# Performance work log

Hardware: AMD Instinct MI355X
Metric: run time of the kernel (lower is better)

The kernel has to match this reference:

```python
import jax, jax.numpy as jnp
import numpy as np

S, B, C = 7, 2, 20
N = B * 5 + C  # 30
L_COORD, L_NOOBJ = 5.0, 0.5


def setup_inputs() -> dict:
    key = jax.random.key(0)
    k1, k2, k3, k4 = jax.random.split(key, 4)
    batch = 16384
    pred = jax.random.uniform(k1, (batch, S, S, N), dtype=jnp.float32)
    target = jax.random.uniform(k2, (batch, S, S, N), dtype=jnp.float32)
    # rescale w/h channels of both boxes to [0.5, 1) so the (buggy) in-place
    # coordinate transform never yields negative values under sqrt
    wh_idx = jnp.array([2, 3, 7, 8])
    pred = pred.at[..., wh_idx].set(0.5 + 0.5 * pred[..., wh_idx])
    target = target.at[..., wh_idx].set(0.5 + 0.5 * target[..., wh_idx])
    obj = jax.random.uniform(k3, (batch, S, S)) < 0.25
    conf = 0.1 + 0.9 * jax.random.uniform(k4, (batch, S, S))
    target = target.at[..., 4].set(jnp.where(obj, conf, 0.0))
    return {"pred": pred, "target": target}


def _yolo_loss(pred, target):
    # Faithful vectorization of the original loop-y torch forward, bugs included:
    #  * x2y2 is computed from the ALREADY transformed xy (xy_new/S + 0.5*wh)
    #  * lambda_coord only multiplies the x / sqrt(w) terms, not y / sqrt(h)
    #  * the selected per-cell loss SUMS l1+l2+l3+IoU (IoU itself is added)
    #  * only the first min(S^2, #coord_cells) coord cells (global flatten
    #    order across the batch) contribute to bbox_loss
    #  * class-prob loss slices dim1 of a [M,2,5] tensor with 10: -> empty -> 0
    p = pred.reshape(-1, N)   # [M, 30], M = b*S*S, row-major like torch mask gather
    t = target.reshape(-1, N)
    obj = t[:, 4] > 0
    rank = jnp.cumsum(obj.astype(jnp.int32)) - 1  # rank among coord cells
    active = obj & (rank < S * S)                 # cells whose bbox loss counts

    pb = p[:, :10].reshape(-1, B, 5)  # [M, B, 5]
    tb = t[:, :10].reshape(-1, B, 5)

    def transform(box):
        xy = box[..., :2] / S - 0.5 * box[..., 2:4]      # new x1,y1
        x2y2 = xy / S + 0.5 * box[..., 2:4]              # uses NEW xy (original bug)
        return xy, x2y2

    pxy, p2 = transform(pb)
    txy, t2 = transform(tb)

    l1 = L_COORD * (txy[..., 0] - pxy[..., 0]) ** 2 + (txy[..., 1] - pxy[..., 1]) ** 2
    l2 = (L_COORD * (jnp.sqrt(t2[..., 0]) - jnp.sqrt(p2[..., 0])) ** 2
          + (jnp.sqrt(t2[..., 1]) - jnp.sqrt(p2[..., 1])) ** 2)
    l3 = (tb[..., 4] - pb[..., 4]) ** 2

    # IoU between pred box j and target box j (boxes as [x1,y1,x2,y2])
    lt = jnp.maximum(pxy, txy)
    rb = jnp.minimum(p2, t2)
    wh = jnp.maximum(rb - lt, 0.0)
    inter = wh[..., 0] * wh[..., 1]
    area_p = (p2[..., 0] - pxy[..., 0]) * (p2[..., 1] - pxy[..., 1])
    area_t = (t2[..., 0] - txy[..., 0]) * (t2[..., 1] - txy[..., 1])
    iou = inter / (area_p + area_t - inter)  # [M, B]

    tot = l1 + l2 + l3 + iou                 # sum(info[argmax]) includes IoU
    jstar = jnp.argmax(iou, axis=1)          # responsible box per cell
    sel = jnp.take_along_axis(tot, jstar[:, None], axis=1)[:, 0]
    bbox_loss = jnp.sum(jnp.where(active, sel, 0.0))

    # no-object confidence loss over both boxes' conf channels (4 and 9)
    noobj = ~obj
    conf_sq = (p[:, 4] - t[:, 4]) ** 2 + (p[:, 9] - t[:, 9]) ** 2
    noobj_loss = L_NOOBJ * jnp.sum(jnp.where(noobj, conf_sq, 0.0))

    # class prob loss: original slices [:, 10:] on a [M, B, 5] tensor -> empty -> 0
    class_prob_loss = jnp.float32(0.0)

    return bbox_loss + noobj_loss + class_prob_loss


def reference(pred, target):
    return _yolo_loss(pred, target)
```

## Files before the change

kernel.cpp:

```cpp
#include <hip/hip_runtime.h>

#define NCH 30
#define RANK_LIMIT 49
#define L_COORD 5.0f
#define L_NOOBJ 0.5f

#define NB 980
#define UNROLL 4
#define OUTER 6
#define CHUNK (256 * UNROLL)
#define NBLK_TOTAL (NB + 1)

typedef float vfloat4 __attribute__((ext_vector_type(4)));

__device__ inline float block_reduce(float v) {
    #pragma unroll
    for (int off = 32; off > 0; off >>= 1)
        v += __shfl_down(v, off, 64);
    __shared__ float s[4];
    int lane = threadIdx.x & 63, wid = threadIdx.x >> 6;
    if (lane == 0) s[wid] = v;
    __syncthreads();
    return (threadIdx.x == 0) ? (s[0] + s[1] + s[2] + s[3]) : 0.0f;
}

__device__ inline float sel_loss(const float* __restrict__ p,
                                 const float* __restrict__ t, int row) {
    const float invS = 1.0f / 7.0f;
    int b0 = row * NCH;
    float tot0 = 0.f, tot1 = 0.f, iou0 = 0.f, iou1 = 0.f;
    #pragma unroll
    for (int j = 0; j < 2; ++j) {
        int o = b0 + 5 * j;
        float px = p[o + 0], py = p[o + 1], pw = p[o + 2], ph = p[o + 3], pc = p[o + 4];
        float tx = t[o + 0], ty = t[o + 1], tw = t[o + 2], th = t[o + 3], tc = t[o + 4];
        float pxy0 = px * invS - 0.5f * pw;
        float pxy1 = py * invS - 0.5f * ph;
        float p2x  = pxy0 * invS + 0.5f * pw;
        float p2y  = pxy1 * invS + 0.5f * ph;
        float txy0 = tx * invS - 0.5f * tw;
        float txy1 = ty * invS - 0.5f * th;
        float t2x  = txy0 * invS + 0.5f * tw;
        float t2y  = txy1 * invS + 0.5f * th;
        float d0 = txy0 - pxy0, d1 = txy1 - pxy1;
        float l1 = L_COORD * d0 * d0 + d1 * d1;
        float s0 = sqrtf(t2x) - sqrtf(p2x);
        float s1 = sqrtf(t2y) - sqrtf(p2y);
        float l2 = L_COORD * s0 * s0 + s1 * s1;
        float dc = tc - pc;
        float l3 = dc * dc;
        float ltx = fmaxf(pxy0, txy0), lty = fmaxf(pxy1, txy1);
        float rbx = fminf(p2x, t2x),   rby = fminf(p2y, t2y);
        float wx  = fmaxf(rbx - ltx, 0.0f);
        float wy  = fmaxf(rby - lty, 0.0f);
        float inter  = wx * wy;
        float area_p = (p2x - pxy0) * (p2y - pxy1);
        float area_t = (t2x - txy0) * (t2y - txy1);
        float io = inter / (area_p + area_t - inter);
        float tt = l1 + l2 + l3 + io;
        if (j == 0) { iou0 = io; tot0 = tt; }
        else        { iou1 = io; tot1 = tt; }
    }
    return (iou1 > iou0) ? tot1 : tot0;
}

__global__ __launch_bounds__(256) void yolo_kernel(const vfloat4* __restrict__ pv,
                                                   const vfloat4* __restrict__ tv,
                                                   const float* __restrict__ ps,
                                                   const float* __restrict__ ts,
                                                   float* __restrict__ partials,
                                                   int M) {
    const int tid  = threadIdx.x;
    const int lane = tid & 63;

    if (blockIdx.x < NB) {
        float s_acc = 0.0f;
        int base = blockIdx.x * CHUNK + tid;
        const int step = NB * CHUNK;

        for (int outer = 0; outer < OUTER; ++outer, base += step) {
            vfloat4 vp[UNROLL], vt[UNROLL];
            #pragma unroll
            for (int u = 0; u < UNROLL; ++u) {
                int i = base + u * 256;
                vp[u] = __builtin_nontemporal_load(&pv[i]);
                vt[u] = __builtin_nontemporal_load(&tv[i]);
            }

            #pragma unroll
            for (int u = 0; u < UNROLL; ++u) {
                int i = base + u * 256;
                int pair = i / 15;
                int k = i - pair * 15;

                float gx = __shfl_up(vt[u].x, 1, 64);
                float gz = __shfl_up(vt[u].z, 1, 64);
                if (lane == 0) {
                    if (k == 2) gx = ts[pair * 60 + 4];
                    if (k == 9) gz = ts[pair * 60 + 34];
                }

                float d1 = vp[u].x - vt[u].x;
                float d2 = vp[u].y - vt[u].y;
                float d8 = vp[u].z - vt[u].z;
                float d9 = vp[u].w - vt[u].w;

                float c1 = (!(vt[u].x > 0.0f)) ? d1 * d1 : 0.0f;
                float c2 = (!(gx      > 0.0f)) ? d2 * d2 : 0.0f;
                float c8 = (!(vt[u].z > 0.0f)) ? d8 * d8 : 0.0f;
                float c9 = (!(gz      > 0.0f)) ? d9 * d9 : 0.0f;

                s_acc += (k == 1) ? c1 : (k == 2) ? c2 : (k == 8) ? c8
                       : (k == 9) ? c9 : 0.0f;
            }
        }

        float part = block_reduce(s_acc);
        if (tid == 0) partials[blockIdx.x] = L_NOOBJ * part;
    } else {
        __shared__ int s_wcnt[4];
        __shared__ int s_base;
        if (tid == 0) s_base = 0;
        __syncthreads();

        float local = 0.0f;
        for (int start = 0; start < M; start += 256) {
            int row = start + tid;
            bool obj = false;
            if (row < M) obj = ts[row * NCH + 4] > 0.0f;

            unsigned long long mask = __ballot(obj);
            int wid = tid >> 6;
            if (lane == 0) s_wcnt[wid] = __popcll(mask);
            __syncthreads();

            int base = s_base;
            int off = 0;
            for (int w = 0; w < wid; ++w) off += s_wcnt[w];
            int rank = base + off + __popcll(mask & ((1ULL << lane) - 1ULL));
            if (obj && rank < RANK_LIMIT) local += sel_loss(ps, ts, row);
            __syncthreads();

            if (tid == 0)
                s_base = base + s_wcnt[0] + s_wcnt[1] + s_wcnt[2] + s_wcnt[3];
            __syncthreads();
            if (s_base >= RANK_LIMIT) break;
        }

        float part = block_reduce(local);
        if (tid == 0) partials[NB] = part;
    }
}

__global__ __launch_bounds__(256) void sum_kernel(const float* __restrict__ partials,
                                                  float* __restrict__ out) {
    float v = 0.0f;
    for (int i = threadIdx.x; i < NBLK_TOTAL; i += 256)
        v += partials[i];
    float tot = block_reduce(v);
    if (threadIdx.x == 0) out[0] = tot;
}

extern "C" void kernel_launch(void* const* d_in, const int* in_sizes, int n_in,
                              void* d_out, int out_size, void* d_ws, size_t ws_size,
                              hipStream_t stream) {
    const float* pred = (const float*)d_in[0];
    const float* targ = (const float*)d_in[1];
    float* out = (float*)d_out;
    float* partials = (float*)d_ws;

    int M = in_sizes[0] / NCH;

    yolo_kernel<<<NBLK_TOTAL, 256, 0, stream>>>(
        (const vfloat4*)pred, (const vfloat4*)targ, pred, targ, partials, M);
    sum_kernel<<<1, 256, 0, stream>>>(partials, out);
}
```

Baseline: 192.0 us.

## Gather only confidence channels for no-object loss instead of streaming full tensors

Replaces the full vectorized streaming pass over both tensors, with its shuffle-based channel selection, by direct scalar loads of channels 4, 9, 34 and 39 for each pair of cells. Each thread handles two cell-pairs and the grid is resized to cover all pairs exactly. The aim is to cut the bytes read and the per-element index arithmetic. The trade-off is strided, poorly coalesced loads that may still pull whole cache lines.

```diff
diff --git a/kernel.cpp b/kernel.cpp
--- a/kernel.cpp
+++ b/kernel.cpp
@@ -5,13 +5,9 @@
 #define L_COORD 5.0f
 #define L_NOOBJ 0.5f
 
-#define NB 980
-#define UNROLL 4
-#define OUTER 6
-#define CHUNK (256 * UNROLL)
+#define NB 784
+#define GPT 2
 #define NBLK_TOTAL (NB + 1)
-
-typedef float vfloat4 __attribute__((ext_vector_type(4)));
 
 __device__ inline float block_reduce(float v) {
     #pragma unroll
@@ -64,9 +60,7 @@
     return (iou1 > iou0) ? tot1 : tot0;
 }
 
-__global__ __launch_bounds__(256) void yolo_kernel(const vfloat4* __restrict__ pv,
-                                                   const vfloat4* __restrict__ tv,
-                                                   const float* __restrict__ ps,
+__global__ __launch_bounds__(256) void yolo_kernel(const float* __restrict__ ps,
                                                    const float* __restrict__ ts,
                                                    float* __restrict__ partials,
                                                    int M) {
@@ -74,48 +68,34 @@
     const int lane = tid & 63;
 
     if (blockIdx.x < NB) {
-        float s_acc = 0.0f;
-        int base = blockIdx.x * CHUNK + tid;
-        const int step = NB * CHUNK;
+        const int g0 = blockIdx.x * (GPT * 256) + tid;
 
-        for (int outer = 0; outer < OUTER; ++outer, base += step) {
-            vfloat4 vp[UNROLL], vt[UNROLL];
-            #pragma unroll
-            for (int u = 0; u < UNROLL; ++u) {
-                int i = base + u * 256;
-                vp[u] = __builtin_nontemporal_load(&pv[i]);
-                vt[u] = __builtin_nontemporal_load(&tv[i]);
-            }
+        float t4[GPT], t9[GPT], t34[GPT], t39[GPT];
+        float p4[GPT], p9[GPT], p34[GPT], p39[GPT];
 
-            #pragma unroll
-            for (int u = 0; u < UNROLL; ++u) {
-                int i = base + u * 256;
-                int pair = i / 15;
-                int k = i - pair * 15;
-
-                float gx = __shfl_up(vt[u].x, 1, 64);
-                float gz = __shfl_up(vt[u].z, 1, 64);
-                if (lane == 0) {
-                    if (k == 2) gx = ts[pair * 60 + 4];
-                    if (k == 9) gz = ts[pair * 60 + 34];
-                }
-
-                float d1 = vp[u].x - vt[u].x;
-                float d2 = vp[u].y - vt[u].y;
-                float d8 = vp[u].z - vt[u].z;
-                float d9 = vp[u].w - vt[u].w;
-
-                float c1 = (!(vt[u].x > 0.0f)) ? d1 * d1 : 0.0f;
-                float c2 = (!(gx      > 0.0f)) ? d2 * d2 : 0.0f;
-                float c8 = (!(vt[u].z > 0.0f)) ? d8 * d8 : 0.0f;
-                float c9 = (!(gz      > 0.0f)) ? d9 * d9 : 0.0f;
-
-                s_acc += (k == 1) ? c1 : (k == 2) ? c2 : (k == 8) ? c8
-                       : (k == 9) ? c9 : 0.0f;
-            }
+        #pragma unroll
+        for (int u = 0; u < GPT; ++u) {
+            const int base = (g0 + u * 256) * 60;
+            const float* tp = ts + base;
+            const float* pp = ps + base;
+            t4[u]  = tp[4];  t9[u]  = tp[9];
+            t34[u] = tp[34]; t39[u] = tp[39];
+            p4[u]  = pp[4];  p9[u]  = pp[9];
+            p34[u] = pp[34]; p39[u] = pp[39];
         }
 
-        float part = block_reduce(s_acc);
+        float acc = 0.0f;
+        #pragma unroll
+        for (int u = 0; u < GPT; ++u) {
+            float d4  = p4[u]  - t4[u];
+            float d9  = p9[u]  - t9[u];
+            float d34 = p34[u] - t34[u];
+            float d39 = p39[u] - t39[u];
+            acc += (t4[u]  > 0.0f) ? 0.0f : (d4 * d4 + d9 * d9);
+            acc += (t34[u] > 0.0f) ? 0.0f : (d34 * d34 + d39 * d39);
+        }
+
+        float part = block_reduce(acc);
         if (tid == 0) partials[blockIdx.x] = L_NOOBJ * part;
     } else {
         __shared__ int s_wcnt[4];
@@ -171,7 +151,6 @@
 
     int M = in_sizes[0] / NCH;
 
-    yolo_kernel<<<NBLK_TOTAL, 256, 0, stream>>>(
-        (const vfloat4*)pred, (const vfloat4*)targ, pred, targ, partials, M);
+    yolo_kernel<<<NBLK_TOTAL, 256, 0, stream>>>(pred, targ, partials, M);
     sum_kernel<<<1, 256, 0, stream>>>(partials, out);
 }
```

After: 211.0 us. 1.1x slower.
